# Performance work log

Measured on AMD Instinct MI355X. Metric: run time of the kernel, lower is better.

Reference implementation:

```python
import jax, jax.numpy as jnp
import numpy as np

W, H, C = 4096, 4096, 3


def setup_inputs() -> dict:
    key = jax.random.key(0)
    k_img, k_perm = jax.random.split(key)
    image = jax.random.normal(k_img, (W, H, C), dtype=jnp.float32)
    # Per-pixel random permutation of channels: argsort of iid uniforms along C
    # reproduces np.random.permutation(c) at every (i, j) deterministically.
    noise = jax.random.uniform(k_perm, (W, H, C))
    perm = jnp.argsort(noise, axis=-1).astype(jnp.int32)  # [W, H, C]
    return {"image": image, "perm": perm}


def reference(image, perm):
    # out[i, j, k] = image[i, j, perm[i, j, k]]  (per-pixel channel gather)
    return jnp.take_along_axis(image, perm, axis=-1)
```

## Files before the change

kernel.cpp:

```cpp
#include <hip/hip_runtime.h>


typedef float f32x2 __attribute__((ext_vector_type(2)));
typedef float f32x4 __attribute__((ext_vector_type(4)));
typedef int   i32x4 __attribute__((ext_vector_type(4)));

#define ITERS 3

__device__ __forceinline__ float sel8(float c0, float c1, float c2, float c3,
                                      float c4, float c5, float c6, float c7,
                                      int idx) {
    float s01 = (idx & 1) ? c1 : c0;
    float s23 = (idx & 1) ? c3 : c2;
    float s45 = (idx & 1) ? c5 : c4;
    float s67 = (idx & 1) ? c7 : c6;
    float s03 = (idx & 2) ? s23 : s01;
    float s47 = (idx & 2) ? s67 : s45;
    return (idx & 4) ? s47 : s03;
}

__global__ __launch_bounds__(256) void PerPixelChannelPermutation_kernel(
    const float* __restrict__ img, const i32x4* __restrict__ perm4,
    f32x4* __restrict__ out4, int nchunks, int n_elems) {
    const int tid = threadIdx.x;
    const int c0  = blockIdx.x * (256 * ITERS) + tid;
    if (c0 >= nchunks) return;

    const f32x4* img4 = (const f32x4*)img;

    f32x4 v[ITERS];
    f32x2 lo[ITERS];
    f32x2 hi[ITERS];
    i32x4 q[ITERS];

#pragma unroll
    for (int i = 0; i < ITERS; ++i) {
        int c = c0 + i * 256;
        if (c >= nchunks) c = c0;
        const int c4 = c * 4;
        v[i] = img4[c];
        int bl = c4 - 2; if (bl < 0) bl = 0;
        int bh = c4 + 4; if (bh > n_elems - 2) bh = n_elems - 2;
        lo[i] = *(const f32x2*)(img + bl);
        hi[i] = *(const f32x2*)(img + bh);
        q[i]  = perm4[c];
    }

    const int p0 = c0 % 3;
#pragma unroll
    for (int i = 0; i < ITERS; ++i) {
        const int c = c0 + i * 256;
        int p = p0 + i;
        if (p >= 3) p -= 3;

        const int off0 = 2 - p;
        const int off3 = 5 - p;
        const int off1 = (p == 0) ? 2 : ((p == 1) ? 1 : 3);
        const int off2 = (p == 0) ? 2 : ((p == 1) ? 4 : 3);

        f32x4 o;
        o.x = sel8(lo[i].x, lo[i].y, v[i].x, v[i].y, v[i].z, v[i].w,
                   hi[i].x, hi[i].y, off0 + q[i].x);
        o.y = sel8(lo[i].x, lo[i].y, v[i].x, v[i].y, v[i].z, v[i].w,
                   hi[i].x, hi[i].y, off1 + q[i].y);
        o.z = sel8(lo[i].x, lo[i].y, v[i].x, v[i].y, v[i].z, v[i].w,
                   hi[i].x, hi[i].y, off2 + q[i].z);
        o.w = sel8(lo[i].x, lo[i].y, v[i].x, v[i].y, v[i].z, v[i].w,
                   hi[i].x, hi[i].y, off3 + q[i].w);

        if (c < nchunks) {
            __builtin_nontemporal_store(o, &out4[c]);
        }
    }
}

extern "C" void kernel_launch(void* const* d_in, const int* in_sizes, int n_in,
                              void* d_out, int out_size, void* d_ws, size_t ws_size,
                              hipStream_t stream) {
    const float* img   = (const float*)d_in[0];
    const i32x4* perm4 = (const i32x4*)d_in[1];
    f32x4*       out4  = (f32x4*)d_out;

    const int n_elems = in_sizes[0];
    const int nchunks = n_elems / 4;

    const int block = 256;
    const int per_block = block * ITERS;
    const int grid = (nchunks + per_block - 1) / per_block;
    PerPixelChannelPermutation_kernel<<<grid, block, 0, stream>>>(
        img, perm4, out4, nchunks, n_elems);
}
```

Before: 449.4 us.

## Fetch neighbour channels via wave shuffles instead of overlapping global loads

Each thread now loads only its own 16-byte chunk and gets the two preceding and two following floats from adjacent lanes with shuffles. Only the first and last lanes of each wave issue extra scalar global loads for the boundary values. Block size rises to 1024 with two chunks per thread, and stores become regular instead of nontemporal. This is meant to cut redundant memory requests, at the cost of cross-lane ops and divergent boundary loads.

```diff
diff --git a/kernel.cpp b/kernel.cpp
--- a/kernel.cpp
+++ b/kernel.cpp
@@ -1,11 +1,11 @@
 #include <hip/hip_runtime.h>
 
 
-typedef float f32x2 __attribute__((ext_vector_type(2)));
 typedef float f32x4 __attribute__((ext_vector_type(4)));
 typedef int   i32x4 __attribute__((ext_vector_type(4)));
 
-#define ITERS 3
+#define ITERS 2
+#define BLOCK 1024
 
 __device__ __forceinline__ float sel8(float c0, float c1, float c2, float c3,
                                       float c4, float c5, float c6, float c7,
@@ -19,37 +19,60 @@
     return (idx & 4) ? s47 : s03;
 }
 
-__global__ __launch_bounds__(256) void PerPixelChannelPermutation_kernel(
+__global__ __launch_bounds__(BLOCK) void PerPixelChannelPermutation_kernel(
     const float* __restrict__ img, const i32x4* __restrict__ perm4,
     f32x4* __restrict__ out4, int nchunks, int n_elems) {
     const int tid = threadIdx.x;
-    const int c0  = blockIdx.x * (256 * ITERS) + tid;
+    const int c0  = blockIdx.x * (BLOCK * ITERS) + tid;
     if (c0 >= nchunks) return;
 
     const f32x4* img4 = (const f32x4*)img;
 
     f32x4 v[ITERS];
-    f32x2 lo[ITERS];
-    f32x2 hi[ITERS];
     i32x4 q[ITERS];
+    int   cc[ITERS];
 
 #pragma unroll
     for (int i = 0; i < ITERS; ++i) {
-        int c = c0 + i * 256;
-        if (c >= nchunks) c = c0;
-        const int c4 = c * 4;
-        v[i] = img4[c];
-        int bl = c4 - 2; if (bl < 0) bl = 0;
-        int bh = c4 + 4; if (bh > n_elems - 2) bh = n_elems - 2;
-        lo[i] = *(const f32x2*)(img + bl);
-        hi[i] = *(const f32x2*)(img + bh);
-        q[i]  = perm4[c];
+        int c = c0 + i * BLOCK;
+        cc[i] = c;
+        int cl = (c < nchunks) ? c : (nchunks - 1);
+        v[i] = img4[cl];
+        q[i] = perm4[cl];
+    }
+
+    float pm2[ITERS], pm1[ITERS], nx0[ITERS], nx1[ITERS];
+#pragma unroll
+    for (int i = 0; i < ITERS; ++i) {
+        pm2[i] = __shfl_up(v[i].z, 1);
+        pm1[i] = __shfl_up(v[i].w, 1);
+        nx0[i] = __shfl_down(v[i].x, 1);
+        nx1[i] = __shfl_down(v[i].y, 1);
+    }
+
+    const int lane = tid & 63;
+    if (lane == 0) {
+#pragma unroll
+        for (int i = 0; i < ITERS; ++i) {
+            int cl = (cc[i] < nchunks) ? cc[i] : (nchunks - 1);
+            int b = cl * 4 - 2; if (b < 0) b = 0;
+            pm2[i] = img[b];
+            pm1[i] = img[b + 1];
+        }
+    }
+    if (lane == 63) {
+#pragma unroll
+        for (int i = 0; i < ITERS; ++i) {
+            int cl = (cc[i] < nchunks) ? cc[i] : (nchunks - 1);
+            int b = cl * 4 + 4; if (b > n_elems - 2) b = n_elems - 2;
+            nx0[i] = img[b];
+            nx1[i] = img[b + 1];
+        }
     }
 
     const int p0 = c0 % 3;
 #pragma unroll
     for (int i = 0; i < ITERS; ++i) {
-        const int c = c0 + i * 256;
         int p = p0 + i;
         if (p >= 3) p -= 3;
 
@@ -59,18 +82,16 @@
         const int off2 = (p == 0) ? 2 : ((p == 1) ? 4 : 3);
 
         f32x4 o;
-        o.x = sel8(lo[i].x, lo[i].y, v[i].x, v[i].y, v[i].z, v[i].w,
-                   hi[i].x, hi[i].y, off0 + q[i].x);
-        o.y = sel8(lo[i].x, lo[i].y, v[i].x, v[i].y, v[i].z, v[i].w,
-                   hi[i].x, hi[i].y, off1 + q[i].y);
-        o.z = sel8(lo[i].x, lo[i].y, v[i].x, v[i].y, v[i].z, v[i].w,
-                   hi[i].x, hi[i].y, off2 + q[i].z);
-        o.w = sel8(lo[i].x, lo[i].y, v[i].x, v[i].y, v[i].z, v[i].w,
-                   hi[i].x, hi[i].y, off3 + q[i].w);
+        o.x = sel8(pm2[i], pm1[i], v[i].x, v[i].y, v[i].z, v[i].w,
+                   nx0[i], nx1[i], off0 + q[i].x);
+        o.y = sel8(pm2[i], pm1[i], v[i].x, v[i].y, v[i].z, v[i].w,
+                   nx0[i], nx1[i], off1 + q[i].y);
+        o.z = sel8(pm2[i], pm1[i], v[i].x, v[i].y, v[i].z, v[i].w,
+                   nx0[i], nx1[i], off2 + q[i].z);
+        o.w = sel8(pm2[i], pm1[i], v[i].x, v[i].y, v[i].z, v[i].w,
+                   nx0[i], nx1[i], off3 + q[i].w);
 
-        if (c < nchunks) {
-            __builtin_nontemporal_store(o, &out4[c]);
-        }
+        if (cc[i] < nchunks) out4[cc[i]] = o;
     }
 }
 
@@ -84,9 +105,8 @@
     const int n_elems = in_sizes[0];
     const int nchunks = n_elems / 4;
 
-    const int block = 256;
-    const int per_block = block * ITERS;
+    const int per_block = BLOCK * ITERS;
     const int grid = (nchunks + per_block - 1) / per_block;
-    PerPixelChannelPermutation_kernel<<<grid, block, 0, stream>>>(
+    PerPixelChannelPermutation_kernel<<<grid, BLOCK, 0, stream>>>(
         img, perm4, out4, nchunks, n_elems);
 }
```

Result: no change. 444.1 us (-1.2%).

## Share neighbor chunks via LDS instead of redundant halo global loads

Applied to the files above, without the earlier changes.

Replaces the per-thread lo/hi 8-byte halo loads with a shared-memory exchange: each thread stores its 16-byte chunk to LDS and reads its neighbours' chunks, and only the edge threads of a block load halo elements from global. The aim is to cut redundant global load instructions and partial-cacheline traffic. In exchange it adds a __syncthreads and drops the 3-chunk-per-thread batching, the bounds check and the nontemporal store. It also assumes nchunks divides evenly by the block size.

```diff
diff --git a/kernel.cpp b/kernel.cpp
--- a/kernel.cpp
+++ b/kernel.cpp
@@ -1,11 +1,10 @@
 #include <hip/hip_runtime.h>
 
 
-typedef float f32x2 __attribute__((ext_vector_type(2)));
 typedef float f32x4 __attribute__((ext_vector_type(4)));
 typedef int   i32x4 __attribute__((ext_vector_type(4)));
 
-#define ITERS 3
+#define BLOCK 256
 
 __device__ __forceinline__ float sel8(float c0, float c1, float c2, float c3,
                                       float c4, float c5, float c6, float c7,
@@ -19,59 +18,58 @@
     return (idx & 4) ? s47 : s03;
 }
 
-__global__ __launch_bounds__(256) void PerPixelChannelPermutation_kernel(
+__global__ __launch_bounds__(BLOCK) void PerPixelChannelPermutation_kernel(
     const float* __restrict__ img, const i32x4* __restrict__ perm4,
     f32x4* __restrict__ out4, int nchunks, int n_elems) {
+    __shared__ f32x4 sv[BLOCK];
+
     const int tid = threadIdx.x;
-    const int c0  = blockIdx.x * (256 * ITERS) + tid;
-    if (c0 >= nchunks) return;
+    const int c   = blockIdx.x * BLOCK + tid;
+    const int c4  = c * 4;
 
     const f32x4* img4 = (const f32x4*)img;
 
-    f32x4 v[ITERS];
-    f32x2 lo[ITERS];
-    f32x2 hi[ITERS];
-    i32x4 q[ITERS];
+    const f32x4 v  = img4[c];
+    const i32x4 qq = perm4[c];
 
-#pragma unroll
-    for (int i = 0; i < ITERS; ++i) {
-        int c = c0 + i * 256;
-        if (c >= nchunks) c = c0;
-        const int c4 = c * 4;
-        v[i] = img4[c];
-        int bl = c4 - 2; if (bl < 0) bl = 0;
-        int bh = c4 + 4; if (bh > n_elems - 2) bh = n_elems - 2;
-        lo[i] = *(const f32x2*)(img + bl);
-        hi[i] = *(const f32x2*)(img + bh);
-        q[i]  = perm4[c];
+    float e0 = 0.f, e1 = 0.f;
+    if (tid == 0) {
+        int b = c4 - 2; if (b < 0) b = 0;
+        e0 = img[b];
+        e1 = img[b + 1];
+    }
+    if (tid == BLOCK - 1) {
+        int b = c4 + 4; if (b > n_elems - 2) b = n_elems - 2;
+        e0 = img[b];
+        e1 = img[b + 1];
     }
 
-    const int p0 = c0 % 3;
-#pragma unroll
-    for (int i = 0; i < ITERS; ++i) {
-        const int c = c0 + i * 256;
-        int p = p0 + i;
-        if (p >= 3) p -= 3;
+    sv[tid] = v;
+    __syncthreads();
 
-        const int off0 = 2 - p;
-        const int off3 = 5 - p;
-        const int off1 = (p == 0) ? 2 : ((p == 1) ? 1 : 3);
-        const int off2 = (p == 0) ? 2 : ((p == 1) ? 4 : 3);
+    const int il = (tid == 0)         ? 0         : tid - 1;
+    const int ih = (tid == BLOCK - 1) ? BLOCK - 1 : tid + 1;
+    const f32x4 L = sv[il];
+    const f32x4 H = sv[ih];
 
-        f32x4 o;
-        o.x = sel8(lo[i].x, lo[i].y, v[i].x, v[i].y, v[i].z, v[i].w,
-                   hi[i].x, hi[i].y, off0 + q[i].x);
-        o.y = sel8(lo[i].x, lo[i].y, v[i].x, v[i].y, v[i].z, v[i].w,
-                   hi[i].x, hi[i].y, off1 + q[i].y);
-        o.z = sel8(lo[i].x, lo[i].y, v[i].x, v[i].y, v[i].z, v[i].w,
-                   hi[i].x, hi[i].y, off2 + q[i].z);
-        o.w = sel8(lo[i].x, lo[i].y, v[i].x, v[i].y, v[i].z, v[i].w,
-                   hi[i].x, hi[i].y, off3 + q[i].w);
+    float pm2 = L.z, pm1 = L.w;
+    float nx0 = H.x, nx1 = H.y;
+    if (tid == 0)         { pm2 = e0; pm1 = e1; }
+    if (tid == BLOCK - 1) { nx0 = e0; nx1 = e1; }
 
-        if (c < nchunks) {
-            __builtin_nontemporal_store(o, &out4[c]);
-        }
-    }
+    const int p = c % 3;
+    const int off0 = 2 - p;
+    const int off3 = 5 - p;
+    const int off1 = (p == 0) ? 2 : ((p == 1) ? 1 : 3);
+    const int off2 = (p == 0) ? 2 : ((p == 1) ? 4 : 3);
+
+    f32x4 o;
+    o.x = sel8(pm2, pm1, v.x, v.y, v.z, v.w, nx0, nx1, off0 + qq.x);
+    o.y = sel8(pm2, pm1, v.x, v.y, v.z, v.w, nx0, nx1, off1 + qq.y);
+    o.z = sel8(pm2, pm1, v.x, v.y, v.z, v.w, nx0, nx1, off2 + qq.z);
+    o.w = sel8(pm2, pm1, v.x, v.y, v.z, v.w, nx0, nx1, off3 + qq.w);
+
+    out4[c] = o;
 }
 
 extern "C" void kernel_launch(void* const* d_in, const int* in_sizes, int n_in,
@@ -84,9 +82,7 @@
     const int n_elems = in_sizes[0];
     const int nchunks = n_elems / 4;
 
-    const int block = 256;
-    const int per_block = block * ITERS;
-    const int grid = (nchunks + per_block - 1) / per_block;
-    PerPixelChannelPermutation_kernel<<<grid, block, 0, stream>>>(
+    const int grid = nchunks / BLOCK;
+    PerPixelChannelPermutation_kernel<<<grid, BLOCK, 0, stream>>>(
         img, perm4, out4, nchunks, n_elems);
 }
```

After: 432.5 us. -3.8%, faster.
